# Performance work log

Hardware: AMD Instinct MI355X
Metric: run time of the kernel (lower is better)

Reference implementation:

```python
import jax, jax.numpy as jnp
import numpy as np

EPS = 1e-6
B, N_NEG, H, D = 256, 1000, 3, 128
NUM_CLUSTER = (25000, 2500, 250)
NUM_IMG = 100000

def _l2norm(x):
    # matches torch F.normalize(dim=-1): x / max(||x||, 1e-12)
    n = jnp.sqrt(jnp.sum(x * x, axis=-1, keepdims=True))
    return x / jnp.maximum(n, 1e-12)

def setup_inputs() -> dict:
    key = jax.random.key(0)
    ks = jax.random.split(key, 10)
    return {
        "semantic_embs": jax.random.normal(ks[0], (B, H * D), dtype=jnp.float32),
        "centroids0": jax.random.normal(ks[1], (NUM_CLUSTER[0], D), dtype=jnp.float32),
        "centroids1": jax.random.normal(ks[2], (NUM_CLUSTER[1], D), dtype=jnp.float32),
        "centroids2": jax.random.normal(ks[3], (NUM_CLUSTER[2], D), dtype=jnp.float32),
        "im2cluster0": jax.random.randint(ks[4], (NUM_IMG,), 0, NUM_CLUSTER[0], dtype=jnp.int32),
        "im2cluster1": jax.random.randint(ks[5], (NUM_IMG,), 0, NUM_CLUSTER[1], dtype=jnp.int32),
        "im2cluster2": jax.random.randint(ks[6], (NUM_IMG,), 0, NUM_CLUSTER[2], dtype=jnp.int32),
        "index": jax.random.randint(ks[7], (B,), 0, NUM_IMG, dtype=jnp.int32),
        "neg_im2cluster": jax.random.randint(ks[8], (B, N_NEG, H), 0, min(NUM_CLUSTER), dtype=jnp.int32),
    }

def reference(semantic_embs, centroids0, centroids1, centroids2,
              im2cluster0, im2cluster1, im2cluster2, index, neg_im2cluster):
    cents = [centroids0, centroids1, centroids2]
    i2c = [im2cluster0, im2cluster1, im2cluster2]
    b = semantic_embs.shape[0]
    se = _l2norm(semantic_embs.reshape(b, H, D))                 # [B,H,D]

    # positive path: gather centroid of each sample's cluster per hierarchy
    pos = jnp.stack([_l2norm(cents[h][i2c[h][index]]) for h in range(H)], axis=1)  # [B,H,D]
    pos_path_sim = jnp.prod((jnp.sum(se * pos, axis=-1) + 1.0) * 0.5, axis=1)      # [B]
    pos_loss = -jnp.log(pos_path_sim + EPS)                                        # [B]

    # negative paths: gather sampled centroids per hierarchy
    neg = jnp.stack([_l2norm(cents[h][neg_im2cluster[:, :, h]]) for h in range(H)], axis=2)  # [B,N,H,D]
    neg_proto_sim = jnp.sum(se[:, None, :, :] * neg, axis=-1)                      # [B,N,H]
    neg_path_sim = jnp.prod((neg_proto_sim + 1.0) * 0.5, axis=-1)                  # [B,N]
    neg_loss = -jnp.log(1.0 - neg_path_sim + EPS)                                  # [B,N]

    # true_negative mask: neg path differs from positive path in any hierarchy
    pos_lab = jnp.stack([i2c[h][index] for h in range(H)], axis=-1)                # [B,H]
    tn = jnp.any(neg_im2cluster != pos_lab[:, None, :], axis=-1).astype(se.dtype)  # [B,N]
    neg_loss = jnp.sum(neg_loss * tn, axis=-1) / (jnp.sum(tn, axis=-1) + EPS)      # [B]

    return jnp.mean(jnp.stack([pos_loss, neg_loss], axis=-1))
```

## Files before the change

### kernel.cpp

```cpp
#include <hip/hip_runtime.h>
#include <math.h>

#define EPS   1e-6f
#define BB    256
#define NNEG  1000
#define HH    3
#define DD    128
#define NCN   250

#define OFF_CENT_T   0

__global__ void kA_prep(const float* __restrict__ c0,
                        const float* __restrict__ c1,
                        const float* __restrict__ c2,
                        float* __restrict__ centT,
                        float* __restrict__ out) {
    if (blockIdx.x == 0 && threadIdx.x == 0) out[0] = 0.0f;
    int wid  = blockIdx.x * 4 + (threadIdx.x >> 6);
    int lane = threadIdx.x & 63;
    if (wid >= HH * NCN) return;
    int h = (wid >= 2 * NCN) ? 2 : (wid >= NCN ? 1 : 0);
    int c = wid - h * NCN;
    const float* cp = (h == 0) ? c0 : (h == 1) ? c1 : c2;
    const float2 v = *(const float2*)(cp + (size_t)c * DD + lane * 2);
    float ss = v.x * v.x + v.y * v.y;
    #pragma unroll
    for (int off = 32; off; off >>= 1) ss += __shfl_xor(ss, off);
    float inv = 1.0f / fmaxf(sqrtf(ss), 1e-12f);
    float* base = centT + h * (DD * NCN);
    base[(lane * 2)     * NCN + c] = v.x * inv;
    base[(lane * 2 + 1) * NCN + c] = v.y * inv;
}

__global__ __launch_bounds__(256) void kB_main(
        const float* __restrict__ se,
        const float* __restrict__ c0,
        const float* __restrict__ c1,
        const float* __restrict__ c2,
        const int* __restrict__ i2c0,
        const int* __restrict__ i2c1,
        const int* __restrict__ i2c2,
        const int* __restrict__ index,
        const int* __restrict__ negc,
        const float* __restrict__ centT,
        float* __restrict__ out) {
    int b = blockIdx.x;
    int tid = threadIdx.x, wave = tid >> 6, lane = tid & 63;

    __shared__ float sse[HH * DD];
    __shared__ float ssim[HH * NCN];
    __shared__ int   slab[HH];
    __shared__ float ph[HH];
    __shared__ float wL[4], wT[4];

    if (wave < HH) {
        int h = wave;
        const float2 s = *(const float2*)(se + (size_t)b * (HH * DD) + h * DD + lane * 2);
        float ss = s.x * s.x + s.y * s.y;
        #pragma unroll
        for (int off = 32; off; off >>= 1) ss += __shfl_xor(ss, off);
        float inv = 1.0f / fmaxf(sqrtf(ss), 1e-12f);
        float2 sn = make_float2(s.x * inv, s.y * inv);
        sse[h * DD + lane * 2]     = sn.x;
        sse[h * DD + lane * 2 + 1] = sn.y;

        int idx = index[b];
        const int*   ip = (h == 0) ? i2c0 : (h == 1) ? i2c1 : i2c2;
        const float* cp = (h == 0) ? c0   : (h == 1) ? c1   : c2;
        int cidx = ip[idx];
        const float2 cv = *(const float2*)(cp + (size_t)cidx * DD + lane * 2);
        float dot = sn.x * cv.x + sn.y * cv.y;
        float csq = cv.x * cv.x + cv.y * cv.y;
        #pragma unroll
        for (int off = 32; off; off >>= 1) {
            dot += __shfl_xor(dot, off);
            csq += __shfl_xor(csq, off);
        }
        if (lane == 0) {
            float invc = 1.0f / fmaxf(sqrtf(csq), 1e-12f);
            ph[h]   = (dot * invc + 1.0f) * 0.5f;
            slab[h] = cidx;
        }
    }
    __syncthreads();

    for (int j = tid; j < HH * NCN; j += 256) {
        int h = (j >= 2 * NCN) ? 2 : (j >= NCN ? 1 : 0);
        int c = j - h * NCN;
        const float* ct = centT + h * (DD * NCN) + c;
        const float* sh = sse + h * DD;
        float acc = 0.0f;
        #pragma unroll 8
        for (int d = 0; d < DD; ++d) acc = fmaf(sh[d], ct[d * NCN], acc);
        ssim[j] = (acc + 1.0f) * 0.5f;
    }
    __syncthreads();

    int l0 = slab[0], l1 = slab[1], l2 = slab[2];
    float accL = 0.0f, accT = 0.0f;
    for (int n = tid; n < NNEG; n += 256) {
        const int* q = negc + ((size_t)b * NNEG + n) * HH;
        int i0 = q[0], i1 = q[1], i2 = q[2];
        float p = ssim[i0] * ssim[NCN + i1] * ssim[2 * NCN + i2];
        if (i0 != l0 || i1 != l1 || i2 != l2) {
            accL -= logf(1.0f - p + EPS);
            accT += 1.0f;
        }
    }
    #pragma unroll
    for (int off = 32; off; off >>= 1) {
        accL += __shfl_xor(accL, off);
        accT += __shfl_xor(accT, off);
    }
    if (lane == 0) { wL[wave] = accL; wT[wave] = accT; }
    __syncthreads();

    if (tid == 0) {
        float L = wL[0] + wL[1] + wL[2] + wL[3];
        float T = wT[0] + wT[1] + wT[2] + wT[3];
        float neg_b = L / (T + EPS);
        float pos_b = -logf(ph[0] * ph[1] * ph[2] + EPS);
        atomicAdd(out, (pos_b + neg_b) * (1.0f / (2.0f * BB)));
    }
}

extern "C" void kernel_launch(void* const* d_in, const int* in_sizes, int n_in,
                              void* d_out, int out_size, void* d_ws, size_t ws_size,
                              hipStream_t stream) {
    const float* se    = (const float*)d_in[0];
    const float* c0    = (const float*)d_in[1];
    const float* c1    = (const float*)d_in[2];
    const float* c2    = (const float*)d_in[3];
    const int*   i2c0  = (const int*)d_in[4];
    const int*   i2c1  = (const int*)d_in[5];
    const int*   i2c2  = (const int*)d_in[6];
    const int*   index = (const int*)d_in[7];
    const int*   negc  = (const int*)d_in[8];

    float* centT = (float*)d_ws + OFF_CENT_T;
    float* out   = (float*)d_out;

    hipLaunchKernelGGL(kA_prep, dim3((HH * NCN + 3) / 4), dim3(256), 0, stream,
                       c0, c1, c2, centT, out);
    hipLaunchKernelGGL(kB_main, dim3(BB), dim3(256), 0, stream,
                       se, c0, c1, c2, i2c0, i2c1, i2c2, index, negc, centT, out);
}
```

Baseline: 100.4 us.

## Fuse centroid prep and main loss into one cooperative kernel with grid sync

Merges the centroid-normalise/transpose kernel into the main per-sample kernel: each block normalises a slice of centroids, then all blocks meet at a cooperative grid-wide sync before reading the transposed table. This removes one kernel launch and the gap between the two kernels. The negative-cluster indices for each sample are copied into shared memory with vectorised int4 loads, replacing strided global loads. The similarity loop now has each thread compute one centroid column across all three hierarchies. The cost is the cooperative-launch overhead and grid-sync latency, plus a requirement that all 256 blocks fit on the device at the same time.

New measurement: 165.6 us. 1.65x slower.

```diff
diff --git a/kernel.cpp b/kernel.cpp
--- a/kernel.cpp
+++ b/kernel.cpp
@@ -1,5 +1,8 @@
 #include <hip/hip_runtime.h>
+#include <hip/hip_cooperative_groups.h>
 #include <math.h>
+
+namespace cg = cooperative_groups;
 
 #define EPS   1e-6f
 #define BB    256
@@ -8,31 +11,7 @@
 #define DD    128
 #define NCN   250
 
-#define OFF_CENT_T   0
-
-__global__ void kA_prep(const float* __restrict__ c0,
-                        const float* __restrict__ c1,
-                        const float* __restrict__ c2,
-                        float* __restrict__ centT,
-                        float* __restrict__ out) {
-    if (blockIdx.x == 0 && threadIdx.x == 0) out[0] = 0.0f;
-    int wid  = blockIdx.x * 4 + (threadIdx.x >> 6);
-    int lane = threadIdx.x & 63;
-    if (wid >= HH * NCN) return;
-    int h = (wid >= 2 * NCN) ? 2 : (wid >= NCN ? 1 : 0);
-    int c = wid - h * NCN;
-    const float* cp = (h == 0) ? c0 : (h == 1) ? c1 : c2;
-    const float2 v = *(const float2*)(cp + (size_t)c * DD + lane * 2);
-    float ss = v.x * v.x + v.y * v.y;
-    #pragma unroll
-    for (int off = 32; off; off >>= 1) ss += __shfl_xor(ss, off);
-    float inv = 1.0f / fmaxf(sqrtf(ss), 1e-12f);
-    float* base = centT + h * (DD * NCN);
-    base[(lane * 2)     * NCN + c] = v.x * inv;
-    base[(lane * 2 + 1) * NCN + c] = v.y * inv;
-}
-
-__global__ __launch_bounds__(256) void kB_main(
+__global__ __launch_bounds__(256, 1) void k_fused(
         const float* __restrict__ se,
         const float* __restrict__ c0,
         const float* __restrict__ c1,
@@ -42,24 +21,50 @@
         const int* __restrict__ i2c2,
         const int* __restrict__ index,
         const int* __restrict__ negc,
-        const float* __restrict__ centT,
+        float* __restrict__ centT,
         float* __restrict__ out) {
     int b = blockIdx.x;
     int tid = threadIdx.x, wave = tid >> 6, lane = tid & 63;
 
     __shared__ float sse[HH * DD];
     __shared__ float ssim[HH * NCN];
+    __shared__ int   snegc[NNEG * HH];
     __shared__ int   slab[HH];
     __shared__ float ph[HH];
     __shared__ float wL[4], wT[4];
 
+    {
+        const int4* src = (const int4*)(negc + (size_t)b * (NNEG * HH));
+        int4* dst = (int4*)snegc;
+        #pragma unroll
+        for (int i = tid; i < (NNEG * HH) / 4; i += 256) dst[i] = src[i];
+    }
+
+    {
+        int wid = b * 4 + wave;
+        if (wid < HH * NCN) {
+            int h = (wid >= 2 * NCN) ? 2 : (wid >= NCN ? 1 : 0);
+            int c = wid - h * NCN;
+            const float* cp = (h == 0) ? c0 : (h == 1) ? c1 : c2;
+            const float2 v = *(const float2*)(cp + (size_t)c * DD + lane * 2);
+            float ssq = v.x * v.x + v.y * v.y;
+            #pragma unroll
+            for (int off = 32; off; off >>= 1) ssq += __shfl_xor(ssq, off);
+            float inv = 1.0f / fmaxf(sqrtf(ssq), 1e-12f);
+            float* base = centT + h * (DD * NCN);
+            base[(lane * 2)     * NCN + c] = v.x * inv;
+            base[(lane * 2 + 1) * NCN + c] = v.y * inv;
+        }
+        if (b == 0 && tid == 0) out[0] = 0.0f;
+    }
+
     if (wave < HH) {
         int h = wave;
         const float2 s = *(const float2*)(se + (size_t)b * (HH * DD) + h * DD + lane * 2);
-        float ss = s.x * s.x + s.y * s.y;
+        float ssq = s.x * s.x + s.y * s.y;
         #pragma unroll
-        for (int off = 32; off; off >>= 1) ss += __shfl_xor(ss, off);
-        float inv = 1.0f / fmaxf(sqrtf(ss), 1e-12f);
+        for (int off = 32; off; off >>= 1) ssq += __shfl_xor(ssq, off);
+        float inv = 1.0f / fmaxf(sqrtf(ssq), 1e-12f);
         float2 sn = make_float2(s.x * inv, s.y * inv);
         sse[h * DD + lane * 2]     = sn.x;
         sse[h * DD + lane * 2 + 1] = sn.y;
@@ -82,25 +87,31 @@
             slab[h] = cidx;
         }
     }
-    __syncthreads();
 
-    for (int j = tid; j < HH * NCN; j += 256) {
-        int h = (j >= 2 * NCN) ? 2 : (j >= NCN ? 1 : 0);
-        int c = j - h * NCN;
-        const float* ct = centT + h * (DD * NCN) + c;
-        const float* sh = sse + h * DD;
-        float acc = 0.0f;
+    __threadfence();
+    cg::this_grid().sync();
+
+    if (tid < NCN) {
+        const float* ct0 = centT + 0 * (DD * NCN) + tid;
+        const float* ct1 = centT + 1 * (DD * NCN) + tid;
+        const float* ct2 = centT + 2 * (DD * NCN) + tid;
+        float a0 = 0.0f, a1 = 0.0f, a2 = 0.0f;
         #pragma unroll 8
-        for (int d = 0; d < DD; ++d) acc = fmaf(sh[d], ct[d * NCN], acc);
-        ssim[j] = (acc + 1.0f) * 0.5f;
+        for (int d = 0; d < DD; ++d) {
+            a0 = fmaf(sse[d],          ct0[(size_t)d * NCN], a0);
+            a1 = fmaf(sse[DD + d],     ct1[(size_t)d * NCN], a1);
+            a2 = fmaf(sse[2 * DD + d], ct2[(size_t)d * NCN], a2);
+        }
+        ssim[tid]           = (a0 + 1.0f) * 0.5f;
+        ssim[NCN + tid]     = (a1 + 1.0f) * 0.5f;
+        ssim[2 * NCN + tid] = (a2 + 1.0f) * 0.5f;
     }
     __syncthreads();
 
     int l0 = slab[0], l1 = slab[1], l2 = slab[2];
     float accL = 0.0f, accT = 0.0f;
     for (int n = tid; n < NNEG; n += 256) {
-        const int* q = negc + ((size_t)b * NNEG + n) * HH;
-        int i0 = q[0], i1 = q[1], i2 = q[2];
+        int i0 = snegc[n * 3], i1 = snegc[n * 3 + 1], i2 = snegc[n * 3 + 2];
         float p = ssim[i0] * ssim[NCN + i1] * ssim[2 * NCN + i2];
         if (i0 != l0 || i1 != l1 || i2 != l2) {
             accL -= logf(1.0f - p + EPS);
@@ -137,11 +148,14 @@
     const int*   index = (const int*)d_in[7];
     const int*   negc  = (const int*)d_in[8];
 
-    float* centT = (float*)d_ws + OFF_CENT_T;
+    float* centT = (float*)d_ws;
     float* out   = (float*)d_out;
 
-    hipLaunchKernelGGL(kA_prep, dim3((HH * NCN + 3) / 4), dim3(256), 0, stream,
-                       c0, c1, c2, centT, out);
-    hipLaunchKernelGGL(kB_main, dim3(BB), dim3(256), 0, stream,
-                       se, c0, c1, c2, i2c0, i2c1, i2c2, index, negc, centT, out);
+    void* args[] = {
+        (void*)&se, (void*)&c0, (void*)&c1, (void*)&c2,
+        (void*)&i2c0, (void*)&i2c1, (void*)&i2c2,
+        (void*)&index, (void*)&negc, (void*)&centT, (void*)&out
+    };
+    hipLaunchCooperativeKernel((const void*)k_fused, dim3(BB), dim3(256),
+                               args, 0, stream);
 }
```
